# Kernel optimization log

Measured on AMD Instinct MI355X. Metric: run time of the kernel, lower is better.

Reference implementation:

```python
import jax, jax.numpy as jnp
import numpy as np
import math

B, C_GT, H, W = 32, 1, 256, 1216
SH, SW = 16, 48  # samplesH, samplesW (eval-mode jitter fixed at 0)


def _gauss_kernel():
    # kernel_size = [int(2H/(SH+1)), int(2W/(SW+1))], sigma = size/3 (per original code)
    kh = int(2 * H / (SH + 1))
    kw = int(2 * W / (SW + 1))
    sh = 2 * H / (SH + 1) / 3.0
    sw = 2 * W / (SW + 1) / 3.0
    gh = np.exp(-(((np.arange(kh) - (kh - 1) / 2) / sh) ** 2) / 2) / (sh * math.sqrt(2 * math.pi))
    gw = np.exp(-(((np.arange(kw) - (kw - 1) / 2) / sw) ** 2) / 2) / (sw * math.sqrt(2 * math.pi))
    k = np.outer(gh, gw)
    k = k / k.sum()
    return jnp.asarray(k, jnp.float32)


def _grid_sample_bilinear(img, grid):
    # img [B,C,H,W]; grid [B,Hs,Ws,2] with (x,y) in [-1,1].
    # Matches F.grid_sample(mode='bilinear', padding_mode='zeros', align_corners=False).
    Bb, C, Hh, Ww = img.shape
    x = (grid[..., 0] + 1.0) * Ww / 2.0 - 0.5
    y = (grid[..., 1] + 1.0) * Hh / 2.0 - 0.5
    x0 = jnp.floor(x); y0 = jnp.floor(y)
    x1 = x0 + 1.0;     y1 = y0 + 1.0
    wx1 = x - x0; wx0 = 1.0 - wx1
    wy1 = y - y0; wy0 = 1.0 - wy1
    imt = img.transpose(0, 2, 3, 1)  # [B,H,W,C]
    bidx = jnp.arange(Bb)[:, None, None]

    def gather(yc, xc, wgt):
        m = (yc >= 0) & (yc <= Hh - 1) & (xc >= 0) & (xc <= Ww - 1)
        yi = jnp.clip(yc, 0, Hh - 1).astype(jnp.int32)
        xi = jnp.clip(xc, 0, Ww - 1).astype(jnp.int32)
        v = imt[bidx, yi, xi]  # [B,Hs,Ws,C]
        return v * (wgt * m)[..., None]

    out = (gather(y0, x0, wy0 * wx0) + gather(y0, x1, wy0 * wx1)
           + gather(y1, x0, wy1 * wx0) + gather(y1, x1, wy1 * wx1))
    return out.transpose(0, 3, 1, 2)  # [B,C,Hs,Ws]


def _forward(gt, dense_vector_field):
    # GaussianSmooth: grouped VALID conv with a big separable Gaussian kernel
    k = _gauss_kernel()
    kern = jnp.broadcast_to(k[None, None], (2, 1, k.shape[0], k.shape[1]))
    smoothed = jax.lax.conv_general_dilated(dense_vector_field, kern, (1, 1), 'VALID',
                                            feature_group_count=2)  # [B,2,H',W']
    # F.interpolate(mode='nearest') to (SH, SW): idx = floor(i * in / out)
    hi = np.arange(SH) * smoothed.shape[2] // SH
    wi = np.arange(SW) * smoothed.shape[3] // SW
    svf = smoothed[:, :, hi][:, :, :, wi]  # [B,2,SH,SW]

    # WarpSample base grid (x first, then y — grid_sample convention)
    gw, gh = np.meshgrid(np.linspace(-(SW - 1) / SW, (SW - 1) / SW, SW),
                         np.linspace(-(SH - 1) / SH, (SH - 1) / SH, SH))
    norm_grid = jnp.asarray(np.stack((gw, gh), 2), jnp.float32)  # [SH,SW,2]
    grid_to_sample = svf.transpose(0, 2, 3, 1) + norm_grid  # [B,SH,SW,2]

    gt_sampled = _grid_sample_bilinear(gt, grid_to_sample)  # [B,1,SH,SW]

    # expand(): vectorized scatter replacing the per-pixel Python loop.
    row = jnp.clip(((grid_to_sample[..., 1] + 1.0) / 2.0 * H).astype(jnp.int32), 0, H - 1)
    col = jnp.clip(((grid_to_sample[..., 0] + 1.0) / 2.0 * W).astype(jnp.int32), 0, W - 1)
    bidx = jnp.arange(gt.shape[0])[:, None, None]
    sparse = jnp.zeros((gt.shape[0], H, W, gt.shape[1]), gt.dtype)
    sparse = sparse.at[bidx, row, col].set(gt_sampled.transpose(0, 2, 3, 1))
    sparse = sparse.transpose(0, 3, 1, 2)  # [B,1,H,W]
    # eval-mode KITTI: zero the top 96 rows (no LiDAR returns there)
    sparse = sparse.at[:, :, 0:96, :].set(0.0)
    return sparse, dense_vector_field.transpose(0, 2, 3, 1), grid_to_sample


def setup_inputs():
    key = jax.random.key(0)
    k1, k2 = jax.random.split(key)
    gt = jax.random.uniform(k1, (B, C_GT, H, W), dtype=jnp.float32) * 80.0  # KITTI depth range
    dense_vector_field = jax.random.normal(k2, (B, 2, H, W), dtype=jnp.float32) * 0.1
    return {"gt": gt, "dense_vector_field": dense_vector_field}


def reference(gt, dense_vector_field):
    return _forward(gt, dense_vector_field)
```

## Files before the change

### kernel.cpp

```cpp
#include <hip/hip_runtime.h>
#include <math.h>

#ifndef M_PI
#define M_PI 3.14159265358979323846
#endif

#define Hh   256
#define Ww   1216
#define HWsz (Hh * Ww)
#define Bb   32
#define KH   30
#define KW   49
#define NTAP (KH * KW)
#define SHs  16
#define SWs  48
#define NPB  (SHs * SWs)
#define NPTS (Bb * NPB)
#define OUT0 (Bb * HWsz)
#define OUT1 (Bb * HWsz * 2)

__device__ __forceinline__ float samp4(const float* __restrict__ g, float yc, float xc, float w) {
#pragma clang fp contract(off)
    bool m = (yc >= 0.0f) && (yc <= 255.0f) && (xc >= 0.0f) && (xc <= 1215.0f);
    float ycl = fminf(fmaxf(yc, 0.0f), 255.0f);
    float xcl = fminf(fmaxf(xc, 0.0f), 1215.0f);
    int yi = (int)ycl, xi = (int)xcl;
    float wm = m ? w : 0.0f;
    return g[yi * Ww + xi] * wm;
}

__global__ __launch_bounds__(256) void k_conv_sample(
    const float* __restrict__ gt, const float* __restrict__ dvf,
    float* __restrict__ out2, float* __restrict__ vbuf, int* __restrict__ rcbuf)
{
#pragma clang fp contract(off)
    __shared__ double s_gh[KH];
    __shared__ double s_gw[KW];
    __shared__ double s_invS;
    __shared__ float  s_w[NTAP];
    const int tid = threadIdx.x;

    if (tid < KH) {
        const double sh_ = (2.0 * 256.0 / 17.0) / 3.0;
        double u = ((double)tid - 14.5) / sh_;
        s_gh[tid] = exp(-(u * u) / 2.0) / (sh_ * sqrt(2.0 * M_PI));
    } else if (tid >= 64 && tid < 64 + KW) {
        int t = tid - 64;
        const double sw_ = (2.0 * 1216.0 / 49.0) / 3.0;
        double u = ((double)t - 24.0) / sw_;
        s_gw[t] = exp(-(u * u) / 2.0) / (sw_ * sqrt(2.0 * M_PI));
    }
    __syncthreads();
    if (tid == 0) {
        double a = 0.0, c = 0.0;
        for (int t = 0; t < KH; ++t) a += s_gh[t];
        for (int t = 0; t < KW; ++t) c += s_gw[t];
        s_invS = 1.0 / (a * c);
    }
    __syncthreads();
    {
        const double invS = s_invS;
        for (int t = tid; t < NTAP; t += 256)
            s_w[t] = (float)((s_gh[t / KW] * s_gw[t % KW]) * invS);
    }
    __syncthreads();

    const int wave = tid >> 6, lane = tid & 63;
    const int pt = blockIdx.x * 4 + wave;
    const int b = pt / NPB, p = pt - b * NPB;
    const int i = p / SWs, j = p - i * SWs;
    const int y0r = (i * 227) >> 4;
    const int x0c = (j * 1168) / 48;
    const float* c0 = dvf + (size_t)b * (2 * HWsz) + y0r * Ww + x0c;
    const float* c1 = c0 + HWsz;

    double a0 = 0.0, a1 = 0.0;
    for (int t = lane; t < NTAP; t += 64) {
        int dy = t / KW, dx = t - dy * KW;
        int off = dy * Ww + dx;
        double w = (double)s_w[t];
        a0 += w * (double)c0[off];
        a1 += w * (double)c1[off];
    }
    for (int o = 32; o > 0; o >>= 1) {
        a0 += __shfl_down(a0, o);
        a1 += __shfl_down(a1, o);
    }

    if (lane == 0) {
        float sx = (float)a0, sy = (float)a1;
        const double startw = -(47.0 / 48.0), stopw = 47.0 / 48.0;
        const double starth = -(15.0 / 16.0), stoph = 15.0 / 16.0;
        const double stepw = (stopw - startw) / 47.0;
        const double steph = (stoph - starth) / 15.0;
        float gwl = (j == SWs - 1) ? (float)stopw : (float)((double)j * stepw + startw);
        float ghl = (i == SHs - 1) ? (float)stoph : (float)((double)i * steph + starth);
        float gx = sx + gwl;
        float gy = sy + ghl;

        float* o2 = out2 + ((size_t)(b * SHs + i) * SWs + j) * 2;
        o2[0] = gx; o2[1] = gy;

        const float* gtb = gt + (size_t)b * HWsz;
        float xw = (gx + 1.0f) * 1216.0f; xw = xw / 2.0f; xw = xw - 0.5f;
        float yw = (gy + 1.0f) * 256.0f;  yw = yw / 2.0f; yw = yw - 0.5f;
        float x0f = floorf(xw), y0f = floorf(yw);
        float x1f = x0f + 1.0f, y1f = y0f + 1.0f;
        float wx1 = xw - x0f, wx0 = 1.0f - wx1;
        float wy1 = yw - y0f, wy0 = 1.0f - wy1;
        float v = samp4(gtb, y0f, x0f, wy0 * wx0) + samp4(gtb, y0f, x1f, wy0 * wx1)
                + samp4(gtb, y1f, x0f, wy1 * wx0) + samp4(gtb, y1f, x1f, wy1 * wx1);

        float rf = (gy + 1.0f) / 2.0f * 256.0f;
        float cf = (gx + 1.0f) / 2.0f * 1216.0f;
        int row = (int)rf; row = row < 0 ? 0 : (row > Hh - 1 ? Hh - 1 : row);
        int col = (int)cf; col = col < 0 ? 0 : (col > Ww - 1 ? Ww - 1 : col);
        vbuf[pt]  = v;
        rcbuf[pt] = (row << 16) | col;
    }
}

__global__ __launch_bounds__(256) void k_scatter(
    const float* __restrict__ vbuf, const int* __restrict__ rcbuf, float* __restrict__ out0)
{
    __shared__ float sv[NPB];
    __shared__ int   sr[NPB];
    const int b = blockIdx.x, tid = threadIdx.x;
    for (int t = tid; t < NPB; t += 256) {
        sv[t] = vbuf[b * NPB + t];
        sr[t] = rcbuf[b * NPB + t];
    }
    __syncthreads();
    float* o = out0 + (size_t)b * HWsz;
    for (int p = tid; p < NPB; p += 256) {
        int rc = sr[p];
        int r = rc >> 16;
        if (r < 96) continue;
        bool win = true;
        for (int q = p + 1; q < NPB; ++q) {
            if (sr[q] == rc) { win = false; break; }
        }
        if (win) o[r * Ww + (rc & 0xffff)] = sv[p];
    }
}

__global__ __launch_bounds__(256) void k_transpose_zero(
    const float* __restrict__ dvf, float* __restrict__ out1, float* __restrict__ out0)
{
    const size_t idx = (size_t)blockIdx.x * 256 + threadIdx.x;
    ((float4*)out0)[idx] = make_float4(0.0f, 0.0f, 0.0f, 0.0f);
    const int b = (int)(idx / (HWsz / 4));
    const int r = (int)(idx - (size_t)b * (HWsz / 4));
    const float4* p0 = (const float4*)(dvf + (size_t)b * 2 * HWsz);
    const float4* p1 = (const float4*)(dvf + (size_t)b * 2 * HWsz + HWsz);
    float4 a = p0[r], c = p1[r];
    float4* o = (float4*)(out1 + ((size_t)b * HWsz + (size_t)r * 4) * 2);
    o[0] = make_float4(a.x, c.x, a.y, c.y);
    o[1] = make_float4(a.z, c.z, a.w, c.w);
}

extern "C" void kernel_launch(void* const* d_in, const int* in_sizes, int n_in,
                              void* d_out, int out_size, void* d_ws, size_t ws_size,
                              hipStream_t stream) {
    const float* gt  = (const float*)d_in[0];
    const float* dvf = (const float*)d_in[1];
    float* out0 = (float*)d_out;
    float* out1 = out0 + OUT0;
    float* out2 = out1 + OUT1;
    float* vbuf  = (float*)d_ws;
    int*   rcbuf = (int*)d_ws + NPTS;

    hipLaunchKernelGGL(k_conv_sample, dim3(NPTS / 4), dim3(256), 0, stream,
                       gt, dvf, out2, vbuf, rcbuf);
    hipLaunchKernelGGL(k_transpose_zero, dim3((Bb * (HWsz / 4)) / 256), dim3(256), 0, stream,
                       dvf, out1, out0);
    hipLaunchKernelGGL(k_scatter, dim3(Bb), dim3(256), 0, stream,
                       vbuf, rcbuf, out0);
}
```

Measured before the change: 298.7 us.

## Stage shared conv window in LDS and precompute Gaussian weights once

The Gaussian weight table moves into a separate single-block kernel that writes it to workspace, so it is no longer recomputed in double precision by every conv block. Each conv block now loads one 30x122 window per channel into LDS, shared by its four adjacent sample points, and the tap loop reads from LDS with a fully unrolled fixed trip count. This cuts redundant global reads from overlapping windows at the cost of an extra launch and about 30KB of LDS per block, which may lower occupancy.

```diff
diff --git a/kernel.cpp b/kernel.cpp
--- a/kernel.cpp
+++ b/kernel.cpp
@@ -19,6 +19,13 @@
 #define OUT0 (Bb * HWsz)
 #define OUT1 (Bb * HWsz * 2)
 
+#define CONV_BLKS (NPTS / 4)
+#define TPOS_BLKS (Bb * (HWsz / 4) / 256)
+
+#define TILE_C 122
+#define TILE_CP 123
+#define STAGE_N (2 * KH * TILE_C)
+
 __device__ __forceinline__ float samp4(const float* __restrict__ g, float yc, float xc, float w) {
 #pragma clang fp contract(off)
     bool m = (yc >= 0.0f) && (yc <= 255.0f) && (xc >= 0.0f) && (xc <= 1215.0f);
@@ -29,15 +36,10 @@
     return g[yi * Ww + xi] * wm;
 }
 
-__global__ __launch_bounds__(256) void k_conv_sample(
-    const float* __restrict__ gt, const float* __restrict__ dvf,
-    float* __restrict__ out2, float* __restrict__ vbuf, int* __restrict__ rcbuf)
-{
-#pragma clang fp contract(off)
+__global__ __launch_bounds__(256) void k_weights(float* __restrict__ wtab) {
     __shared__ double s_gh[KH];
     __shared__ double s_gw[KW];
     __shared__ double s_invS;
-    __shared__ float  s_w[NTAP];
     const int tid = threadIdx.x;
 
     if (tid < KH) {
@@ -58,29 +60,62 @@
         s_invS = 1.0 / (a * c);
     }
     __syncthreads();
-    {
-        const double invS = s_invS;
-        for (int t = tid; t < NTAP; t += 256)
-            s_w[t] = (float)((s_gh[t / KW] * s_gw[t % KW]) * invS);
-    }
+    const double invS = s_invS;
+    for (int t = tid; t < NTAP; t += 256)
+        wtab[t] = (float)((s_gh[t / KW] * s_gw[t % KW]) * invS);
+}
+
+__global__ __launch_bounds__(256) void k_conv(
+    const float* __restrict__ gt, const float* __restrict__ dvf,
+    const float* __restrict__ wtab,
+    float* __restrict__ out2, float* __restrict__ vbuf, int* __restrict__ rcbuf)
+{
+#pragma clang fp contract(off)
+    __shared__ float s_win[2][KH][TILE_CP];
+    __shared__ float s_w[NTAP];
+    const int tid = threadIdx.x;
+
+    const int p0 = blockIdx.x * 4;
+    const int b  = p0 / NPB, pp0 = p0 - b * NPB;
+    const int i  = pp0 / SWs, j0 = pp0 - i * SWs;
+    const int y0r  = (i * 227) >> 4;
+    const int x_min = (j0 * 1168) / 48;
+    const size_t bbase = (size_t)b * (2 * HWsz);
+
+#pragma unroll 4
+    for (int e = tid; e < STAGE_N; e += 256) {
+        int ch  = e / (KH * TILE_C);
+        int rem = e - ch * (KH * TILE_C);
+        int row = rem / TILE_C, col = rem - row * TILE_C;
+        s_win[ch][row][col] = dvf[bbase + (size_t)ch * HWsz + (size_t)(y0r + row) * Ww + x_min + col];
+    }
+#pragma unroll
+    for (int t = tid; t < NTAP; t += 256)
+        s_w[t] = wtab[t];
     __syncthreads();
 
     const int wave = tid >> 6, lane = tid & 63;
-    const int pt = blockIdx.x * 4 + wave;
-    const int b = pt / NPB, p = pt - b * NPB;
-    const int i = p / SWs, j = p - i * SWs;
-    const int y0r = (i * 227) >> 4;
-    const int x0c = (j * 1168) / 48;
-    const float* c0 = dvf + (size_t)b * (2 * HWsz) + y0r * Ww + x0c;
-    const float* c1 = c0 + HWsz;
+    const int j  = j0 + wave;
+    const int pt = p0 + wave;
+    const int xoff = (j * 1168) / 48 - x_min;
 
     double a0 = 0.0, a1 = 0.0;
-    for (int t = lane; t < NTAP; t += 64) {
+#pragma unroll
+    for (int k = 0; k < 22; ++k) {
+        int t = lane + 64 * k;
         int dy = t / KW, dx = t - dy * KW;
-        int off = dy * Ww + dx;
+        int cl = xoff + dx;
         double w = (double)s_w[t];
-        a0 += w * (double)c0[off];
-        a1 += w * (double)c1[off];
+        a0 += w * (double)s_win[0][dy][cl];
+        a1 += w * (double)s_win[1][dy][cl];
+    }
+    if (lane < 62) {
+        int t = lane + 64 * 22;
+        int dy = t / KW, dx = t - dy * KW;
+        int cl = xoff + dx;
+        double w = (double)s_w[t];
+        a0 += w * (double)s_win[0][dy][cl];
+        a1 += w * (double)s_win[1][dy][cl];
     }
     for (int o = 32; o > 0; o >>= 1) {
         a0 += __shfl_down(a0, o);
@@ -120,6 +155,21 @@
     }
 }
 
+__global__ __launch_bounds__(256) void k_tpose(
+    const float* __restrict__ dvf, float* __restrict__ out1, float* __restrict__ out0)
+{
+    const size_t idx = (size_t)blockIdx.x * 256 + threadIdx.x;
+    ((float4*)out0)[idx] = make_float4(0.0f, 0.0f, 0.0f, 0.0f);
+    const int b = (int)(idx / (HWsz / 4));
+    const int rr = (int)(idx - (size_t)b * (HWsz / 4));
+    const float4* p0 = (const float4*)(dvf + (size_t)b * 2 * HWsz);
+    const float4* p1 = (const float4*)(dvf + (size_t)b * 2 * HWsz + HWsz);
+    float4 a = p0[rr], c = p1[rr];
+    float4* o = (float4*)(out1 + ((size_t)b * HWsz + (size_t)rr * 4) * 2);
+    o[0] = make_float4(a.x, c.x, a.y, c.y);
+    o[1] = make_float4(a.z, c.z, a.w, c.w);
+}
+
 __global__ __launch_bounds__(256) void k_scatter(
     const float* __restrict__ vbuf, const int* __restrict__ rcbuf, float* __restrict__ out0)
 {
@@ -144,21 +194,6 @@
     }
 }
 
-__global__ __launch_bounds__(256) void k_transpose_zero(
-    const float* __restrict__ dvf, float* __restrict__ out1, float* __restrict__ out0)
-{
-    const size_t idx = (size_t)blockIdx.x * 256 + threadIdx.x;
-    ((float4*)out0)[idx] = make_float4(0.0f, 0.0f, 0.0f, 0.0f);
-    const int b = (int)(idx / (HWsz / 4));
-    const int r = (int)(idx - (size_t)b * (HWsz / 4));
-    const float4* p0 = (const float4*)(dvf + (size_t)b * 2 * HWsz);
-    const float4* p1 = (const float4*)(dvf + (size_t)b * 2 * HWsz + HWsz);
-    float4 a = p0[r], c = p1[r];
-    float4* o = (float4*)(out1 + ((size_t)b * HWsz + (size_t)r * 4) * 2);
-    o[0] = make_float4(a.x, c.x, a.y, c.y);
-    o[1] = make_float4(a.z, c.z, a.w, c.w);
-}
-
 extern "C" void kernel_launch(void* const* d_in, const int* in_sizes, int n_in,
                               void* d_out, int out_size, void* d_ws, size_t ws_size,
                               hipStream_t stream) {
@@ -169,10 +204,12 @@
     float* out2 = out1 + OUT1;
     float* vbuf  = (float*)d_ws;
     int*   rcbuf = (int*)d_ws + NPTS;
-
-    hipLaunchKernelGGL(k_conv_sample, dim3(NPTS / 4), dim3(256), 0, stream,
-                       gt, dvf, out2, vbuf, rcbuf);
-    hipLaunchKernelGGL(k_transpose_zero, dim3((Bb * (HWsz / 4)) / 256), dim3(256), 0, stream,
+    float* wtab  = (float*)d_ws + 2 * NPTS;
+
+    hipLaunchKernelGGL(k_weights, dim3(1), dim3(256), 0, stream, wtab);
+    hipLaunchKernelGGL(k_conv, dim3(CONV_BLKS), dim3(256), 0, stream,
+                       gt, dvf, wtab, out2, vbuf, rcbuf);
+    hipLaunchKernelGGL(k_tpose, dim3(TPOS_BLKS), dim3(256), 0, stream,
                        dvf, out1, out0);
     hipLaunchKernelGGL(k_scatter, dim3(Bb), dim3(256), 0, stream,
                        vbuf, rcbuf, out0);
```

New measurement: 305.5 us. +2.3%, slower.
